# Performance work log

Measured on AMD Instinct MI355X. Metric: run time of the kernel, lower is better.

## Reference

```python
import jax, jax.numpy as jnp
import numpy as np

# FalconMamba2 SSM decoder layer: RMSNorm -> Mamba2 mixer (in_proj, causal depthwise
# conv + SiLU, chunked SSD scan, gated RMSNorm, out_proj) -> residual add.
H_DIM = 2048      # hidden_size
D_SSM = 4096      # mamba_expand * hidden_size
NH = 64           # num heads
P = 64            # head_dim = D_SSM // NH
G = 1             # n_groups
N = 128           # ssm state size
K = 4             # conv kernel
CS = 256          # chunk size
EPS = 1e-5


def rmsnorm(x, w, eps=EPS):
    v = jnp.mean(jnp.square(x), axis=-1, keepdims=True)
    return x * jax.lax.rsqrt(v + eps) * w


def setup_inputs() -> dict:
    key = jax.random.key(0)
    ks = jax.random.split(key, 8)
    proj_dim = 2 * D_SSM + 2 * G * N + NH   # 8512
    conv_dim = D_SSM + 2 * G * N            # 4352
    s = 0.02
    return {
        "x": jax.random.normal(ks[0], (1, 2048, H_DIM), jnp.float32),
        "rms_w": jnp.ones((H_DIM,), jnp.float32),
        "W_in": jax.random.normal(ks[1], (proj_dim, H_DIM), jnp.float32) * s,
        "conv_w": jax.random.normal(ks[2], (conv_dim, K), jnp.float32) * 0.2,
        "conv_b": jnp.zeros((conv_dim,), jnp.float32),
        "dt_bias": jax.random.uniform(ks[3], (NH,), jnp.float32,
                                      minval=float(np.log(1e-3)), maxval=float(np.log(0.1))),
        "A_log": jnp.log(jax.random.uniform(ks[4], (NH,), jnp.float32, minval=1.0, maxval=16.0)),
        "D": jax.random.normal(ks[5], (NH,), jnp.float32) * 0.1 + 1.0,
        "norm_w": jnp.ones((D_SSM,), jnp.float32),
        "W_out": jax.random.normal(ks[6], (H_DIM, D_SSM), jnp.float32) * s,
    }


def reference(x, rms_w, W_in, conv_w, conv_b, dt_bias, A_log, D, norm_w, W_out):
    Bsz, L, _ = x.shape
    h = rmsnorm(x, rms_w)                                   # input_layernorm
    proj = jnp.einsum('blh,ph->blp', h, W_in)               # in_proj (no bias)
    z, xBC, dt = jnp.split(proj, [D_SSM, 2 * D_SSM + 2 * G * N], axis=-1)

    # causal depthwise conv1d (kernel K) + SiLU
    xp = jnp.pad(xBC, ((0, 0), (K - 1, 0), (0, 0)))
    xc = conv_b + sum(xp[:, k:k + L, :] * conv_w[:, k] for k in range(K))
    xc = jax.nn.silu(xc)
    xs, Bm, Cm = jnp.split(xc, [D_SSM, D_SSM + G * N], axis=-1)

    dt = jax.nn.softplus(dt + dt_bias)                      # [B,L,NH]
    A = -jnp.exp(A_log)                                     # [NH]

    nc = L // CS
    xs = xs.reshape(Bsz, nc, CS, NH, P)
    Bm = Bm.reshape(Bsz, nc, CS, G, N)
    Cm = Cm.reshape(Bsz, nc, CS, G, N)
    dtc = dt.reshape(Bsz, nc, CS, NH)

    dA = dtc * A                                            # [B,c,l,h]
    dAc = jnp.cumsum(dA, axis=2)
    dAh = jnp.moveaxis(dAc, 3, 2)                           # [B,c,h,l]
    dth = jnp.moveaxis(dtc, 3, 2)                           # [B,c,h,l]

    # intra-chunk (diagonal block) output
    seg = dAh[..., :, None] - dAh[..., None, :]             # [B,c,h,l,s]
    tril = jnp.tril(jnp.ones((CS, CS), bool))
    Lmat = jnp.exp(jnp.where(tril, seg, -jnp.inf))
    CB = jnp.einsum('bclgn,bcsgn->bcls', Cm, Bm)            # G=1 shared across heads
    M = CB[:, :, None] * Lmat * dth[..., None, :]           # [B,c,h,l,s]
    Y_diag = jnp.einsum('bchls,bcshp->bclhp', M, xs)

    # per-chunk final states and inter-chunk recurrence
    decay_states = jnp.exp(dAh[..., -1:] - dAh)             # [B,c,h,l]
    states = jnp.einsum('bclgn,bchl,bclhp->bchpn', Bm, decay_states * dth, xs)
    chunk_decay = jnp.exp(dAh[..., -1])                     # [B,c,h]

    def step(carry, inp):
        dec, st = inp
        return carry * dec[..., None, None] + st, carry     # emit state BEFORE chunk

    st_t = jnp.moveaxis(states, 1, 0)                       # [c,B,h,p,n]
    dec_t = jnp.moveaxis(chunk_decay, 1, 0)                 # [c,B,h]
    _, prev_states = jax.lax.scan(step, jnp.zeros_like(st_t[0]), (dec_t, st_t))
    prev_states = jnp.moveaxis(prev_states, 0, 1)           # [B,c,h,p,n]

    Y_off = jnp.einsum('bclgn,bchpn,bchl->bclhp', Cm, prev_states, jnp.exp(dAh))

    y = (Y_diag + Y_off + xs * D[:, None]).reshape(Bsz, L, D_SSM)
    y = rmsnorm(y * jax.nn.silu(z), norm_w)                 # gated RMSNorm
    out = jnp.einsum('bld,hd->blh', y, W_out)               # out_proj
    return x + out                                          # residual
```

## Files before the change

### kernel.cpp

```cpp
#include <hip/hip_runtime.h>
#include <stdint.h>


typedef __bf16 bf16x8 __attribute__((ext_vector_type(8)));
typedef float  f32x4  __attribute__((ext_vector_type(4)));

#define DEVFN __device__ __forceinline__

DEVFN unsigned short f2b(float f) {
  uint32_t u = __builtin_bit_cast(uint32_t, f);
  u += 0x7fffu + ((u >> 16) & 1u);
  return (unsigned short)(u >> 16);
}
DEVFN float b2f(unsigned short u) {
  uint32_t x = (uint32_t)u << 16;
  return __builtin_bit_cast(float, x);
}
DEVFN bf16x8 pack8(const float (&m)[8]) {
  bf16x8 r;
#pragma unroll
  for (int t = 0; t < 8; ++t) r[t] = (__bf16)m[t];
  return r;
}

DEVFN void tile_map(int bid, int nwg, int nm, int nn, int grp, int& mt, int& nt) {
  const int q = nwg >> 3, r = nwg & 7;
  const int xcd = bid & 7, lid = bid >> 3;
  const int wg = (xcd < r ? xcd * (q + 1) : r * (q + 1) + (xcd - r) * q) + lid;
  const int per = grp * nn;
  const int g = wg / per;
  const int rem = wg - g * per;
  const int lim = nm - g * grp;
  const int gm = lim < grp ? lim : grp;
  mt = g * grp + rem % gm;
  nt = rem / gm;
}

__global__ void f32_to_bf16_two(
    const float* __restrict__ s1, unsigned short* __restrict__ d1,
    long src1, long dst1,
    const float* __restrict__ s2, unsigned short* __restrict__ d2,
    long src2, long dst2) {
  long i = ((long)blockIdx.x * 256 + threadIdx.x) * 4;
  const float* s; unsigned short* d; long srcE;
  if (i < dst1) { s = s1; d = d1; srcE = src1; }
  else {
    i -= dst1;
    if (i >= dst2) return;
    s = s2; d = d2; srcE = src2;
  }
  ushort4 o;
  if (i < srcE) {
    float4 v = *reinterpret_cast<const float4*>(s + i);
    o.x = f2b(v.x); o.y = f2b(v.y); o.z = f2b(v.z); o.w = f2b(v.w);
  } else {
    o.x = 0; o.y = 0; o.z = 0; o.w = 0;
  }
  *reinterpret_cast<ushort4*>(d + i) = o;
}

__global__ __launch_bounds__(256) void rmsnorm_in(
    const float* __restrict__ x, const float* __restrict__ w,
    unsigned short* __restrict__ h) {
  const int row = blockIdx.x;
  const int base = threadIdx.x * 8;
  if (row >= 2048) {
    ushort4 z = {0, 0, 0, 0};
    *reinterpret_cast<ushort4*>(h + (size_t)row * 2048 + base)     = z;
    *reinterpret_cast<ushort4*>(h + (size_t)row * 2048 + base + 4) = z;
    return;
  }
  const float* xr = x + (size_t)row * 2048;
  float4 v0 = *reinterpret_cast<const float4*>(xr + base);
  float4 v1 = *reinterpret_cast<const float4*>(xr + base + 4);
  float ss = v0.x*v0.x + v0.y*v0.y + v0.z*v0.z + v0.w*v0.w
           + v1.x*v1.x + v1.y*v1.y + v1.z*v1.z + v1.w*v1.w;
  __shared__ float red[4];
#pragma unroll
  for (int off = 32; off > 0; off >>= 1) ss += __shfl_xor(ss, off);
  if ((threadIdx.x & 63) == 0) red[threadIdx.x >> 6] = ss;
  __syncthreads();
  ss = red[0] + red[1] + red[2] + red[3];
  const float scale = rsqrtf(ss * (1.0f / 2048.0f) + 1e-5f);
  float vals[8] = {v0.x, v0.y, v0.z, v0.w, v1.x, v1.y, v1.z, v1.w};
  unsigned short o[8];
#pragma unroll
  for (int j = 0; j < 8; ++j) o[j] = f2b(vals[j] * scale * w[base + j]);
  ushort4 a, b;
  a.x = o[0]; a.y = o[1]; a.z = o[2]; a.w = o[3];
  b.x = o[4]; b.y = o[5]; b.z = o[6]; b.w = o[7];
  *reinterpret_cast<ushort4*>(h + (size_t)row * 2048 + base)     = a;
  *reinterpret_cast<ushort4*>(h + (size_t)row * 2048 + base + 4) = b;
}

template<int BM, bool RES>
__global__ __launch_bounds__(256, 2) void gemm_pipe(
    const unsigned short* __restrict__ A, const unsigned short* __restrict__ B,
    float* __restrict__ C, const float* __restrict__ res,
    int K, int Mc, int Nc, int ldc, int nm, int nn, int grp) {
  constexpr int MF = BM / 32;
  __shared__ __align__(16) unsigned short As[2][BM * 64];
  __shared__ __align__(16) unsigned short Bs[2][128 * 64];
  int mt, nt;
  tile_map(blockIdx.x, nm * nn, nm, nn, grp, mt, nt);
  const int m0 = mt * BM;
  const int n0 = nt * 128;
  const int tid  = threadIdx.x;
  const int wid  = tid >> 6;
  const int lane = tid & 63;
  const int wm   = (wid >> 1) * (BM / 2);
  const int wn   = (wid & 1) * 64;
  const int lrow = lane & 15;
  const int lkc  = lane >> 4;

  auto stageA = [&](int buf, int k0) {
#pragma unroll
    for (int i = 0; i < MF; ++i) {
      const int ci = tid + i * 256;
      const int r = ci >> 3, cc = ci & 7;
      const int gc = cc ^ (r & 7);
      __builtin_amdgcn_global_load_lds(
          (const __attribute__((address_space(1))) void*)(A + (size_t)(m0 + r) * K + k0 + gc * 8),
          (__attribute__((address_space(3))) void*)(&As[buf][ci * 8]), 16, 0, 0);
    }
  };
  auto stageB = [&](int buf, int k0) {
#pragma unroll
    for (int i = 0; i < 4; ++i) {
      const int ci = tid + i * 256;
      const int r = ci >> 3, cc = ci & 7;
      const int gc = cc ^ (r & 7);
      __builtin_amdgcn_global_load_lds(
          (const __attribute__((address_space(1))) void*)(B + (size_t)(n0 + r) * K + k0 + gc * 8),
          (__attribute__((address_space(3))) void*)(&Bs[buf][ci * 8]), 16, 0, 0);
    }
  };

  f32x4 acc[MF][4] = {};
  const int nsteps = K >> 6;

  stageA(0, 0); stageB(0, 0);
  if (nsteps > 1) { stageA(1, 64); stageB(1, 64); }
  if (nsteps > 1) asm volatile("s_waitcnt vmcnt(%0)" :: "n"(MF + 4) : "memory");
  else            asm volatile("s_waitcnt vmcnt(0)" ::: "memory");
  __builtin_amdgcn_s_barrier();
  __builtin_amdgcn_sched_barrier(0);

  int cur = 0;
  for (int t = 0; t < nsteps; ++t) {
    bf16x8 af[MF][2], bf[4][2];
#pragma unroll
    for (int m = 0; m < MF; ++m)
#pragma unroll
      for (int kk = 0; kk < 2; ++kk) {
        const int row = wm + m * 16 + lrow;
        const int c = kk * 4 + lkc;
        af[m][kk] = *reinterpret_cast<const bf16x8*>(
            &As[cur][row * 64 + ((c ^ (row & 7)) * 8)]);
      }
#pragma unroll
    for (int n = 0; n < 4; ++n)
#pragma unroll
      for (int kk = 0; kk < 2; ++kk) {
        const int row = wn + n * 16 + lrow;
        const int c = kk * 4 + lkc;
        bf[n][kk] = *reinterpret_cast<const bf16x8*>(
            &Bs[cur][row * 64 + ((c ^ (row & 7)) * 8)]);
      }
    asm volatile("s_waitcnt lgkmcnt(0)" ::: "memory");
    __builtin_amdgcn_sched_barrier(0);
    __builtin_amdgcn_s_barrier();
    if (t + 2 < nsteps) { stageA(cur, (t + 2) * 64); stageB(cur, (t + 2) * 64); }
    __builtin_amdgcn_s_setprio(1);
#pragma unroll
    for (int kk = 0; kk < 2; ++kk)
#pragma unroll
      for (int m = 0; m < MF; ++m)
#pragma unroll
        for (int n = 0; n < 4; ++n)
          acc[m][n] = __builtin_amdgcn_mfma_f32_16x16x32_bf16(af[m][kk], bf[n][kk], acc[m][n], 0, 0, 0);
    __builtin_amdgcn_s_setprio(0);
    if (t + 1 < nsteps) {
      if (t + 2 < nsteps) asm volatile("s_waitcnt vmcnt(%0)" :: "n"(MF + 4) : "memory");
      else                asm volatile("s_waitcnt vmcnt(0)" ::: "memory");
      __builtin_amdgcn_sched_barrier(0);
      __builtin_amdgcn_s_barrier();
    }
    cur ^= 1;
  }

#pragma unroll
  for (int m = 0; m < MF; ++m) {
#pragma unroll
    for (int n = 0; n < 4; ++n) {
      const int col = n0 + wn + n * 16 + lrow;
      if (col < Nc) {
#pragma unroll
        for (int v = 0; v < 4; ++v) {
          const int row = m0 + wm + m * 16 + (lane >> 4) * 4 + v;
          if (row < Mc) {
            const size_t idx = (size_t)row * ldc + col;
            float val = acc[m][n][v];
            if (RES) val += res[idx];
            C[idx] = val;
          }
        }
      }
    }
  }
}

template<int BM, bool RES>
__global__ __launch_bounds__(256, 2) void gemm_pipe3(
    const unsigned short* __restrict__ A, const unsigned short* __restrict__ B,
    float* __restrict__ C, const float* __restrict__ res,
    int K, int Mc, int Nc, int ldc, int nm, int nn, int grp) {
  constexpr int MF = BM / 32;
  constexpr int LPS = MF + 4;
  __shared__ __align__(16) unsigned short As[3][BM * 64];
  __shared__ __align__(16) unsigned short Bs[3][128 * 64];
  int mt, nt;
  tile_map(blockIdx.x, nm * nn, nm, nn, grp, mt, nt);
  const int m0 = mt * BM;
  const int n0 = nt * 128;
  const int tid  = threadIdx.x;
  const int wid  = tid >> 6;
  const int lane = tid & 63;
  const int wm   = (wid >> 1) * (BM / 2);
  const int wn   = (wid & 1) * 64;
  const int lrow = lane & 15;
  const int lkc  = lane >> 4;

  auto stage = [&](int buf, int k0) {
#pragma unroll
    for (int i = 0; i < MF; ++i) {
      const int ci = tid + i * 256;
      const int r = ci >> 3, cc = ci & 7;
      const int gc = cc ^ (r & 7);
      __builtin_amdgcn_global_load_lds(
          (const __attribute__((address_space(1))) void*)(A + (size_t)(m0 + r) * K + k0 + gc * 8),
          (__attribute__((address_space(3))) void*)(&As[buf][ci * 8]), 16, 0, 0);
    }
#pragma unroll
    for (int i = 0; i < 4; ++i) {
      const int ci = tid + i * 256;
      const int r = ci >> 3, cc = ci & 7;
      const int gc = cc ^ (r & 7);
      __builtin_amdgcn_global_load_lds(
          (const __attribute__((address_space(1))) void*)(B + (size_t)(n0 + r) * K + k0 + gc * 8),
          (__attribute__((address_space(3))) void*)(&Bs[buf][ci * 8]), 16, 0, 0);
    }
  };

  f32x4 acc[MF][4] = {};
  const int nsteps = K >> 6;

  stage(0, 0);
  if (nsteps > 1) stage(1, 64);
  if (nsteps > 2) stage(2, 128);
  if (nsteps > 2)      asm volatile("s_waitcnt vmcnt(%0)" :: "n"(2 * LPS) : "memory");
  else if (nsteps > 1) asm volatile("s_waitcnt vmcnt(%0)" :: "n"(LPS) : "memory");
  else                 asm volatile("s_waitcnt vmcnt(0)" ::: "memory");
  __builtin_amdgcn_s_barrier();
  __builtin_amdgcn_sched_barrier(0);

  int cur = 0;
  for (int t = 0; t < nsteps; ++t) {
    bf16x8 af[MF][2], bf[4][2];
#pragma unroll
    for (int m = 0; m < MF; ++m)
#pragma unroll
      for (int kk = 0; kk < 2; ++kk) {
        const int row = wm + m * 16 + lrow;
        const int c = kk * 4 + lkc;
        af[m][kk] = *reinterpret_cast<const bf16x8*>(
            &As[cur][row * 64 + ((c ^ (row & 7)) * 8)]);
      }
#pragma unroll
    for (int n = 0; n < 4; ++n)
#pragma unroll
      for (int kk = 0; kk < 2; ++kk) {
        const int row = wn + n * 16 + lrow;
        const int c = kk * 4 + lkc;
        bf[n][kk] = *reinterpret_cast<const bf16x8*>(
            &Bs[cur][row * 64 + ((c ^ (row & 7)) * 8)]);
      }
    asm volatile("s_waitcnt lgkmcnt(0)" ::: "memory");
    __builtin_amdgcn_sched_barrier(0);
    __builtin_amdgcn_s_barrier();
    if (t + 3 < nsteps) stage(cur, (t + 3) * 64);
    __builtin_amdgcn_s_setprio(1);
#pragma unroll
    for (int kk = 0; kk < 2; ++kk)
#pragma unroll
      for (int m = 0; m < MF; ++m)
#pragma unroll
        for (int n = 0; n < 4; ++n)
          acc[m][n] = __builtin_amdgcn_mfma_f32_16x16x32_bf16(af[m][kk], bf[n][kk], acc[m][n], 0, 0, 0);
    __builtin_amdgcn_s_setprio(0);
    if (t + 1 < nsteps) {
      if (t + 3 < nsteps)      asm volatile("s_waitcnt vmcnt(%0)" :: "n"(2 * LPS) : "memory");
      else if (t + 2 < nsteps) asm volatile("s_waitcnt vmcnt(%0)" :: "n"(LPS) : "memory");
      else                     asm volatile("s_waitcnt vmcnt(0)" ::: "memory");
      __builtin_amdgcn_sched_barrier(0);
      __builtin_amdgcn_s_barrier();
    }
    cur = (cur == 2) ? 0 : cur + 1;
  }

#pragma unroll
  for (int m = 0; m < MF; ++m) {
#pragma unroll
    for (int n = 0; n < 4; ++n) {
      const int col = n0 + wn + n * 16 + lrow;
      if (col < Nc) {
#pragma unroll
        for (int v = 0; v < 4; ++v) {
          const int row = m0 + wm + m * 16 + (lane >> 4) * 4 + v;
          if (row < Mc) {
            const size_t idx = (size_t)row * ldc + col;
            float val = acc[m][n][v];
            if (RES) val += res[idx];
            C[idx] = val;
          }
        }
      }
    }
  }
}

__global__ __launch_bounds__(256) void conv_silu_dt(
    const float* __restrict__ proj, const float* __restrict__ conv_w,
    const float* __restrict__ conv_b, const float* __restrict__ dt_bias,
    unsigned short* __restrict__ xs, float* __restrict__ BC,
    unsigned short* __restrict__ BTb, unsigned short* __restrict__ Bsb,
    unsigned short* __restrict__ Cbb, float* __restrict__ dtc) {
  const int cch = blockIdx.x * 256 + threadIdx.x;
  const int l0 = blockIdx.y * 16;
  if (cch < 4352) {
    const float4 w = *reinterpret_cast<const float4*>(conv_w + (size_t)cch * 4);
    const float b = conv_b[cch];
    const float* pcol = proj + 4096 + cch;
    float w0, w1, w2;
    w0 = (l0 >= 3) ? pcol[(size_t)(l0 - 3) * 8512] : 0.0f;
    w1 = (l0 >= 2) ? pcol[(size_t)(l0 - 2) * 8512] : 0.0f;
    w2 = (l0 >= 1) ? pcol[(size_t)(l0 - 1) * 8512] : 0.0f;
#pragma unroll
    for (int i = 0; i < 16; ++i) {
      const int l = l0 + i;
      const float cur = pcol[(size_t)l * 8512];
      float acc = b + w0 * w.x + w1 * w.y + w2 * w.z + cur * w.w;
      w0 = w1; w1 = w2; w2 = cur;
      acc = acc / (1.0f + __expf(-acc));
      if (cch < 4096) {
        xs[(size_t)l * 4096 + cch] = f2b(acc);
      } else {
        BC[(size_t)l * 256 + (cch - 4096)] = acc;
        if (cch < 4224) {
          const int n = cch - 4096;
          const unsigned short bb = f2b(acc);
          BTb[((size_t)((l >> 8) * 128) + n) * 256 + (l & 255)] = bb;
          Bsb[(size_t)l * 128 + n] = bb;
        } else {
          const int n = cch - 4224;
          Cbb[(size_t)l * 128 + n] = f2b(acc);
        }
      }
    }
  } else if (cch < 4416) {
    const int hh = cch - 4352;
    const float bias = dt_bias[hh];
#pragma unroll
    for (int i = 0; i < 16; ++i) {
      const int l = l0 + i;
      const float v = proj[(size_t)l * 8512 + 8448 + hh] + bias;
      dtc[(size_t)l * 64 + hh] = (v > 20.0f) ? v : log1pf(expf(v));
    }
  }
}

__global__ __launch_bounds__(256) void cb_mfma(
    const unsigned short* __restrict__ Cbb,
    const unsigned short* __restrict__ Bsb,
    float* __restrict__ CB) {
  const int bx = blockIdx.x;
  const int c = bx >> 3;
  const int l0 = (bx & 7) * 32;
  const int tid = threadIdx.x;
  const int wid = tid >> 6;
  const int lane = tid & 63;
  const int wm = (wid >> 1) * 16;
  const int wn = (wid & 1) * 128;
  const int lrow = lane & 15;
  const int lk = (lane >> 4) * 8;
  const size_t arow = (size_t)(c * 256 + l0 + wm + lrow) * 128;
  f32x4 acc[8] = {};
#pragma unroll
  for (int kk = 0; kk < 4; ++kk) {
    bf16x8 av = *reinterpret_cast<const bf16x8*>(Cbb + arow + kk * 32 + lk);
#pragma unroll
    for (int nf = 0; nf < 8; ++nf) {
      bf16x8 bv = *reinterpret_cast<const bf16x8*>(
          Bsb + (size_t)(c * 256 + wn + nf * 16 + lrow) * 128 + kk * 32 + lk);
      acc[nf] = __builtin_amdgcn_mfma_f32_16x16x32_bf16(av, bv, acc[nf], 0, 0, 0);
    }
  }
#pragma unroll
  for (int nf = 0; nf < 8; ++nf) {
    const int s = wn + nf * 16 + lrow;
#pragma unroll
    for (int v = 0; v < 4; ++v) {
      const int l = l0 + wm + (lane >> 4) * 4 + v;
      CB[((size_t)(c * 256) + l) * 256 + s] = acc[nf][v];
    }
  }
}

__global__ __launch_bounds__(512) void ssd_states_scan(
    const unsigned short* __restrict__ xs, const unsigned short* __restrict__ BTb,
    const float* __restrict__ dtc, const float* __restrict__ A_log,
    float* __restrict__ dAc, float* __restrict__ cdec,
    float* __restrict__ statesT) {
  const int bx = blockIdx.x;
  const int c = bx >> 6, h = bx & 63;
  __shared__ __align__(16) unsigned short xwT[64 * 264];
  __shared__ float dAL[256], dtL[256];
  const int tid = threadIdx.x;
  const int lane = tid & 63;
  const int w = tid >> 6;

  if (tid < 256) dtL[tid] = dtc[(size_t)(c * 256 + tid) * 64 + h];
  const float Ah = -__expf(A_log[h]);
  __syncthreads();
  if (tid < 256) dAL[tid] = dtL[tid] * Ah;
  __syncthreads();
  for (int off = 1; off < 256; off <<= 1) {
    const float t = (tid < 256 && tid >= off) ? dAL[tid - off] : 0.0f;
    __syncthreads();
    if (tid < 256) dAL[tid] += t;
    __syncthreads();
  }
  if (tid < 256) dAc[(size_t)bx * 256 + tid] = dAL[tid];
  if (tid == 255) cdec[bx] = __expf(dAL[255]);
  if (tid < 256) dtL[tid] = __expf(dAL[255] - dAL[tid]) * dtL[tid];
  __syncthreads();

#pragma unroll
  for (int it = 0; it < 4; ++it) {
    const int gid = it * 512 + tid;
    const int p = gid & 63;
    const int s0 = (gid >> 6) * 8;
    bf16x8 r;
#pragma unroll
    for (int k = 0; k < 8; ++k)
      r[k] = (__bf16)(b2f(xs[(size_t)(c * 256 + s0 + k) * 4096 + h * 64 + p]) * dtL[s0 + k]);
    *reinterpret_cast<bf16x8*>(&xwT[p * 264 + s0]) = r;
  }
  __syncthreads();

  const int pb = (w & 3) * 16;
  const int nb = (w >> 2) * 64;
  const int kcol = (lane >> 4) * 8;
  f32x4 acc[4] = {};
  for (int k = 0; k < 8; ++k) {
    bf16x8 av = *reinterpret_cast<const bf16x8*>(&xwT[(pb + (lane & 15)) * 264 + k * 32 + kcol]);
#pragma unroll
    for (int nf = 0; nf < 4; ++nf) {
      bf16x8 bv = *reinterpret_cast<const bf16x8*>(
          BTb + ((size_t)(c * 128) + nb + nf * 16 + (lane & 15)) * 256 + k * 32 + kcol);
      acc[nf] = __builtin_amdgcn_mfma_f32_16x16x32_bf16(av, bv, acc[nf], 0, 0, 0);
    }
  }
  const int rb = (lane >> 4) * 4;
#pragma unroll
  for (int nf = 0; nf < 4; ++nf) {
    const int n = nb + nf * 16 + (lane & 15);
#pragma unroll
    for (int v = 0; v < 4; ++v) {
      const int p = pb + rb + v;
      statesT[(size_t)bx * 8192 + p * 128 + n] = acc[nf][v];
    }
  }
}

__global__ void ssd_scan(const float* __restrict__ statesT,
                         unsigned short* __restrict__ prevb,
                         const float* __restrict__ cdec) {
  const int i = blockIdx.x * 256 + threadIdx.x;
  const int h = i >> 13;
  const int r = i & 8191;
  float carry = 0.0f;
#pragma unroll
  for (int c = 0; c < 8; ++c) {
    const size_t idx = ((size_t)(c * 64 + h)) * 8192 + r;
    const float st = statesT[idx];
    prevb[idx] = f2b(carry);
    carry = carry * cdec[c * 64 + h] + st;
  }
}

__global__ __launch_bounds__(512) void ssd_diag_off(
    const unsigned short* xs, const float* __restrict__ BC,
    const float* __restrict__ dtc, const float* __restrict__ dAc,
    const float* __restrict__ CB, const unsigned short* __restrict__ prevb,
    const float* __restrict__ Dp, unsigned short* y) {
  const int bx = blockIdx.x;
  const int c = bx >> 6, h = bx & 63;
  __shared__ __align__(16) unsigned short xsT[64 * 264];
  __shared__ float dAL[256], dtL[256], vdt[256];
  const int tid = threadIdx.x;
  const int lane = tid & 63;
  const int w = tid >> 6;

  if (tid < 256) {
    dAL[tid] = dAc[(size_t)bx * 256 + tid];
    dtL[tid] = dtc[(size_t)(c * 256 + tid) * 64 + h];
  }
  __syncthreads();
  if (tid < 256) vdt[tid] = __expf(dAL[tid | 31] - dAL[tid]) * dtL[tid];
#pragma unroll
  for (int it = 0; it < 4; ++it) {
    const int gid = it * 512 + tid;
    const int p = gid & 63;
    const int s0 = (gid >> 6) * 8;
    unsigned short r[8];
#pragma unroll
    for (int k = 0; k < 8; ++k)
      r[k] = xs[(size_t)(c * 256 + s0 + k) * 4096 + h * 64 + p];
    *reinterpret_cast<uint4*>(&xsT[p * 264 + s0]) = *reinterpret_cast<uint4*>(r);
  }
  __syncthreads();

  const int l1 = w * 32 + (lane & 15);
  const int l2 = l1 + 16;
  const int kcol = (lane >> 4) * 8;
  const float dA1 = dAL[l1], dA2 = dAL[l2];
  const float* CBr1 = CB + ((size_t)(c * 256) + l1) * 256;
  const float* CBr2 = CB + ((size_t)(c * 256) + l2) * 256;
  f32x4 acc[2][4] = {};

  for (int j = 0; j < w; ++j) {
    const int s0 = j * 32 + kcol;
    float cb1[8], cb2[8];
    *reinterpret_cast<float4*>(&cb1[0]) = *reinterpret_cast<const float4*>(CBr1 + s0);
    *reinterpret_cast<float4*>(&cb1[4]) = *reinterpret_cast<const float4*>(CBr1 + s0 + 4);
    *reinterpret_cast<float4*>(&cb2[0]) = *reinterpret_cast<const float4*>(CBr2 + s0);
    *reinterpret_cast<float4*>(&cb2[4]) = *reinterpret_cast<const float4*>(CBr2 + s0 + 4);
    const float a = dAL[j * 32 + 31];
    const float u1 = __expf(dA1 - a), u2 = __expf(dA2 - a);
    float m1[8], m2[8];
#pragma unroll
    for (int t = 0; t < 8; ++t) {
      const float uv = vdt[s0 + t];
      m1[t] = cb1[t] * (u1 * uv);
      m2[t] = cb2[t] * (u2 * uv);
    }
    bf16x8 a1 = pack8(m1), a2 = pack8(m2);
#pragma unroll
    for (int nf = 0; nf < 4; ++nf) {
      bf16x8 bv = *reinterpret_cast<const bf16x8*>(
          &xsT[(nf * 16 + (lane & 15)) * 264 + j * 32 + kcol]);
      acc[0][nf] = __builtin_amdgcn_mfma_f32_16x16x32_bf16(a1, bv, acc[0][nf], 0, 0, 0);
      acc[1][nf] = __builtin_amdgcn_mfma_f32_16x16x32_bf16(a2, bv, acc[1][nf], 0, 0, 0);
    }
  }
  {
    const int s0 = w * 32 + kcol;
    float cb1[8], cb2[8];
    *reinterpret_cast<float4*>(&cb1[0]) = *reinterpret_cast<const float4*>(CBr1 + s0);
    *reinterpret_cast<float4*>(&cb1[4]) = *reinterpret_cast<const float4*>(CBr1 + s0 + 4);
    *reinterpret_cast<float4*>(&cb2[0]) = *reinterpret_cast<const float4*>(CBr2 + s0);
    *reinterpret_cast<float4*>(&cb2[4]) = *reinterpret_cast<const float4*>(CBr2 + s0 + 4);
    float m1[8], m2[8];
#pragma unroll
    for (int t = 0; t < 8; ++t) {
      const int s = s0 + t;
      const float e1 = __expf(fminf(dA1 - dAL[s], 0.0f)) * dtL[s];
      const float e2 = __expf(fminf(dA2 - dAL[s], 0.0f)) * dtL[s];
      m1[t] = (s <= l1) ? cb1[t] * e1 : 0.0f;
      m2[t] = (s <= l2) ? cb2[t] * e2 : 0.0f;
    }
    bf16x8 a1 = pack8(m1), a2 = pack8(m2);
#pragma unroll
    for (int nf = 0; nf < 4; ++nf) {
      bf16x8 bv = *reinterpret_cast<const bf16x8*>(
          &xsT[(nf * 16 + (lane & 15)) * 264 + w * 32 + kcol]);
      acc[0][nf] = __builtin_amdgcn_mfma_f32_16x16x32_bf16(a1, bv, acc[0][nf], 0, 0, 0);
      acc[1][nf] = __builtin_amdgcn_mfma_f32_16x16x32_bf16(a2, bv, acc[1][nf], 0, 0, 0);
    }
  }
  {
    const float eA1 = __expf(dA1), eA2 = __expf(dA2);
    const float* Cr1 = BC + ((size_t)(c * 256) + l1) * 256 + 128;
    const float* Cr2 = BC + ((size_t)(c * 256) + l2) * 256 + 128;
    const unsigned short* pv = prevb + (size_t)bx * 8192;
#pragma unroll
    for (int q = 0; q < 4; ++q) {
      const int n0 = q * 32 + kcol;
      float c1[8], c2[8];
      *reinterpret_cast<float4*>(&c1[0]) = *reinterpret_cast<const float4*>(Cr1 + n0);
      *reinterpret_cast<float4*>(&c1[4]) = *reinterpret_cast<const float4*>(Cr1 + n0 + 4);
      *reinterpret_cast<float4*>(&c2[0]) = *reinterpret_cast<const float4*>(Cr2 + n0);
      *reinterpret_cast<float4*>(&c2[4]) = *reinterpret_cast<const float4*>(Cr2 + n0 + 4);
      float m1[8], m2[8];
#pragma unroll
      for (int t = 0; t < 8; ++t) { m1[t] = c1[t] * eA1; m2[t] = c2[t] * eA2; }
      bf16x8 a1 = pack8(m1), a2 = pack8(m2);
#pragma unroll
      for (int nf = 0; nf < 4; ++nf) {
        bf16x8 bv = *reinterpret_cast<const bf16x8*>(
            pv + (size_t)(nf * 16 + (lane & 15)) * 128 + n0);
        acc[0][nf] = __builtin_amdgcn_mfma_f32_16x16x32_bf16(a1, bv, acc[0][nf], 0, 0, 0);
        acc[1][nf] = __builtin_amdgcn_mfma_f32_16x16x32_bf16(a2, bv, acc[1][nf], 0, 0, 0);
      }
    }
  }
  const float Dh = Dp[h];
  const int rb = (lane >> 4) * 4;
#pragma unroll
  for (int mf = 0; mf < 2; ++mf) {
#pragma unroll
    for (int nf = 0; nf < 4; ++nf) {
      const int p = nf * 16 + (lane & 15);
#pragma unroll
      for (int v = 0; v < 4; ++v) {
        const int l = w * 32 + mf * 16 + rb + v;
        y[(size_t)(c * 256 + l) * 4096 + h * 64 + p] =
            f2b(acc[mf][nf][v] + Dh * b2f(xsT[p * 264 + l]));
      }
    }
  }
}

__global__ __launch_bounds__(256) void gated_rmsnorm(
    const unsigned short* __restrict__ y, const float* __restrict__ proj,
    const float* __restrict__ nw, unsigned short* __restrict__ y2) {
  const int row = blockIdx.x;
  const unsigned short* yr = y + (size_t)row * 4096;
  const float* zr = proj + (size_t)row * 8512;
  const int base = threadIdx.x * 16;
  unsigned short yu[16];
  *reinterpret_cast<uint4*>(&yu[0]) = *reinterpret_cast<const uint4*>(yr + base);
  *reinterpret_cast<uint4*>(&yu[8]) = *reinterpret_cast<const uint4*>(yr + base + 8);
  float g[16];
  float ss = 0.0f;
#pragma unroll
  for (int j = 0; j < 16; j += 4) {
    const float4 zv = *reinterpret_cast<const float4*>(zr + base + j);
    const float a0 = b2f(yu[j])     * (zv.x / (1.0f + expf(-zv.x)));
    const float a1 = b2f(yu[j + 1]) * (zv.y / (1.0f + expf(-zv.y)));
    const float a2 = b2f(yu[j + 2]) * (zv.z / (1.0f + expf(-zv.z)));
    const float a3 = b2f(yu[j + 3]) * (zv.w / (1.0f + expf(-zv.w)));
    g[j] = a0; g[j+1] = a1; g[j+2] = a2; g[j+3] = a3;
    ss += a0*a0 + a1*a1 + a2*a2 + a3*a3;
  }
  __shared__ float red[4];
#pragma unroll
  for (int off = 32; off > 0; off >>= 1) ss += __shfl_xor(ss, off);
  if ((threadIdx.x & 63) == 0) red[threadIdx.x >> 6] = ss;
  __syncthreads();
  ss = red[0] + red[1] + red[2] + red[3];
  const float scale = rsqrtf(ss * (1.0f / 4096.0f) + 1e-5f);
#pragma unroll
  for (int j = 0; j < 16; j += 4) {
    ushort4 o;
    o.x = f2b(g[j]   * scale * nw[base + j]);
    o.y = f2b(g[j+1] * scale * nw[base + j + 1]);
    o.z = f2b(g[j+2] * scale * nw[base + j + 2]);
    o.w = f2b(g[j+3] * scale * nw[base + j + 3]);
    *reinterpret_cast<ushort4*>(y2 + (size_t)row * 4096 + base + j) = o;
  }
}

extern "C" void kernel_launch(void* const* d_in, const int* in_sizes, int n_in,
                              void* d_out, int out_size, void* d_ws, size_t ws_size,
                              hipStream_t stream) {
  const float* x       = (const float*)d_in[0];
  const float* rms_w   = (const float*)d_in[1];
  const float* W_in    = (const float*)d_in[2];
  const float* conv_w  = (const float*)d_in[3];
  const float* conv_b  = (const float*)d_in[4];
  const float* dt_bias = (const float*)d_in[5];
  const float* A_log   = (const float*)d_in[6];
  const float* Dp      = (const float*)d_in[7];
  const float* norm_w  = (const float*)d_in[8];
  const float* W_out   = (const float*)d_in[9];
  float* out = (float*)d_out;

  char* ws = (char*)d_ws;
  size_t off = 0;
  auto alloc = [&](size_t bytes) {
    void* p = ws + off;
    off += (bytes + 255) & ~(size_t)255;
    return p;
  };
  unsigned short* Wb_in  = (unsigned short*)alloc((size_t)8576 * 2048 * 2);
  unsigned short* Wb_out = (unsigned short*)alloc((size_t)2048 * 4096 * 2);
  unsigned short* hbuf   = (unsigned short*)alloc((size_t)2112 * 2048 * 2);
  float* proj   = (float*)alloc((size_t)2048 * 8512 * 4);
  unsigned short* xsbuf = (unsigned short*)alloc((size_t)2048 * 4096 * 2);
  float* BCbuf  = (float*)alloc((size_t)2048 * 256 * 4);
  unsigned short* BTb = (unsigned short*)alloc((size_t)8 * 128 * 256 * 2);
  unsigned short* Bsb = (unsigned short*)alloc((size_t)2048 * 128 * 2);
  unsigned short* Cbb = (unsigned short*)alloc((size_t)2048 * 128 * 2);
  float* dtcbuf = (float*)alloc((size_t)2048 * 64 * 4);
  float* dAcbuf = (float*)alloc((size_t)512 * 256 * 4);
  float* cdec   = (float*)alloc((size_t)512 * 4);
  float* CBbuf  = (float*)alloc((size_t)8 * 256 * 256 * 4);
  float* statesT = (float*)alloc((size_t)512 * 64 * 128 * 4);
  unsigned short* y2 = Wb_in;
  unsigned short* prevb = hbuf;

  (void)in_sizes; (void)n_in; (void)out_size; (void)ws_size;

  {
    const long d1 = (long)8576 * 2048, s1 = (long)8512 * 2048;
    const long d2 = (long)2048 * 4096, s2 = d2;
    const long chunks = (d1 + d2) / 4;
    f32_to_bf16_two<<<(int)((chunks + 255) / 256), 256, 0, stream>>>(
        W_in, Wb_in, s1, d1, W_out, Wb_out, s2, d2);
  }

  rmsnorm_in<<<2112, 256, 0, stream>>>(x, rms_w, hbuf);

  gemm_pipe<192, false><<<11 * 67, 256, 0, stream>>>(hbuf, Wb_in, proj, nullptr,
                                                     2048, 2048, 8512, 8512,
                                                     11, 67, 4);

  conv_silu_dt<<<dim3(18, 128), 256, 0, stream>>>(proj, conv_w, conv_b, dt_bias,
                                                  xsbuf, BCbuf, BTb, Bsb, Cbb,
                                                  dtcbuf);

  cb_mfma<<<64, 256, 0, stream>>>(Cbb, Bsb, CBbuf);

  ssd_states_scan<<<512, 512, 0, stream>>>(xsbuf, BTb, dtcbuf, A_log,
                                           dAcbuf, cdec, statesT);

  ssd_scan<<<2048, 256, 0, stream>>>(statesT, prevb, cdec);

  ssd_diag_off<<<512, 512, 0, stream>>>(xsbuf, BCbuf, dtcbuf, dAcbuf, CBbuf,
                                        prevb, Dp, xsbuf);

  gated_rmsnorm<<<2048, 256, 0, stream>>>(xsbuf, proj, norm_w, y2);

  gemm_pipe3<64, true><<<32 * 16, 256, 0, stream>>>(y2, Wb_out, out, x,
                                                    4096, 2048, 2048, 2048,
                                                    32, 16, 4);
}
```

Baseline: 267.9 us.

## Store in_proj output as bf16 and fuse small kernels into neighbors

The in_proj GEMM now writes its projection in bf16 instead of fp32. The conv/dt and gated RMSNorm kernels read that bf16 buffer, which halves traffic on the largest intermediate. Weight conversion and the input RMSNorm are merged into one launch, and the C·B MFMA kernel is folded into the states kernel as extra blocks, cutting launch overhead. The cost is reduced precision for z, xBC and dt before the softplus and conv.

```diff
diff --git a/kernel.cpp b/kernel.cpp
--- a/kernel.cpp
+++ b/kernel.cpp
@@ -36,33 +36,33 @@
   nt = rem / gm;
 }
 
-__global__ void f32_to_bf16_two(
-    const float* __restrict__ s1, unsigned short* __restrict__ d1,
-    long src1, long dst1,
-    const float* __restrict__ s2, unsigned short* __restrict__ d2,
-    long src2, long dst2) {
-  long i = ((long)blockIdx.x * 256 + threadIdx.x) * 4;
-  const float* s; unsigned short* d; long srcE;
-  if (i < dst1) { s = s1; d = d1; srcE = src1; }
-  else {
-    i -= dst1;
-    if (i >= dst2) return;
-    s = s2; d = d2; srcE = src2;
-  }
-  ushort4 o;
-  if (i < srcE) {
-    float4 v = *reinterpret_cast<const float4*>(s + i);
-    o.x = f2b(v.x); o.y = f2b(v.y); o.z = f2b(v.z); o.w = f2b(v.w);
-  } else {
-    o.x = 0; o.y = 0; o.z = 0; o.w = 0;
-  }
-  *reinterpret_cast<ushort4*>(d + i) = o;
-}
-
-__global__ __launch_bounds__(256) void rmsnorm_in(
-    const float* __restrict__ x, const float* __restrict__ w,
-    unsigned short* __restrict__ h) {
-  const int row = blockIdx.x;
+__global__ __launch_bounds__(256) void prep(
+    const float* __restrict__ W_in, unsigned short* __restrict__ Wb_in,
+    const float* __restrict__ W_out, unsigned short* __restrict__ Wb_out,
+    const float* __restrict__ x, const float* __restrict__ rms_w,
+    unsigned short* __restrict__ h, int ncvt) {
+  const long d1 = (long)8576 * 2048, s1 = (long)8512 * 2048;
+  const long d2 = (long)2048 * 4096;
+  if (blockIdx.x < (unsigned)ncvt) {
+    long i = ((long)blockIdx.x * 256 + threadIdx.x) * 4;
+    const float* s; unsigned short* d; long srcE;
+    if (i < d1) { s = W_in; d = Wb_in; srcE = s1; }
+    else {
+      i -= d1;
+      if (i >= d2) return;
+      s = W_out; d = Wb_out; srcE = d2;
+    }
+    ushort4 o;
+    if (i < srcE) {
+      float4 v = *reinterpret_cast<const float4*>(s + i);
+      o.x = f2b(v.x); o.y = f2b(v.y); o.z = f2b(v.z); o.w = f2b(v.w);
+    } else {
+      o.x = 0; o.y = 0; o.z = 0; o.w = 0;
+    }
+    *reinterpret_cast<ushort4*>(d + i) = o;
+    return;
+  }
+  const int row = blockIdx.x - ncvt;
   const int base = threadIdx.x * 8;
   if (row >= 2048) {
     ushort4 z = {0, 0, 0, 0};
@@ -85,7 +85,7 @@
   float vals[8] = {v0.x, v0.y, v0.z, v0.w, v1.x, v1.y, v1.z, v1.w};
   unsigned short o[8];
 #pragma unroll
-  for (int j = 0; j < 8; ++j) o[j] = f2b(vals[j] * scale * w[base + j]);
+  for (int j = 0; j < 8; ++j) o[j] = f2b(vals[j] * scale * rms_w[base + j]);
   ushort4 a, b;
   a.x = o[0]; a.y = o[1]; a.z = o[2]; a.w = o[3];
   b.x = o[4]; b.y = o[5]; b.z = o[6]; b.w = o[7];
@@ -93,10 +93,10 @@
   *reinterpret_cast<ushort4*>(h + (size_t)row * 2048 + base + 4) = b;
 }
 
-template<int BM, bool RES>
+template<int BM, bool RES, bool OUT16>
 __global__ __launch_bounds__(256, 2) void gemm_pipe(
     const unsigned short* __restrict__ A, const unsigned short* __restrict__ B,
-    float* __restrict__ C, const float* __restrict__ res,
+    void* __restrict__ Cv, const float* __restrict__ res,
     int K, int Mc, int Nc, int ldc, int nm, int nn, int grp) {
   constexpr int MF = BM / 32;
   __shared__ __align__(16) unsigned short As[2][BM * 64];
@@ -201,8 +201,12 @@
           if (row < Mc) {
             const size_t idx = (size_t)row * ldc + col;
             float val = acc[m][n][v];
-            if (RES) val += res[idx];
-            C[idx] = val;
+            if constexpr (OUT16) {
+              ((unsigned short*)Cv)[idx] = f2b(val);
+            } else {
+              if (RES) val += res[idx];
+              ((float*)Cv)[idx] = val;
+            }
           }
         }
       }
@@ -330,7 +334,7 @@
 }
 
 __global__ __launch_bounds__(256) void conv_silu_dt(
-    const float* __restrict__ proj, const float* __restrict__ conv_w,
+    const unsigned short* __restrict__ proj, const float* __restrict__ conv_w,
     const float* __restrict__ conv_b, const float* __restrict__ dt_bias,
     unsigned short* __restrict__ xs, float* __restrict__ BC,
     unsigned short* __restrict__ BTb, unsigned short* __restrict__ Bsb,
@@ -340,15 +344,15 @@
   if (cch < 4352) {
     const float4 w = *reinterpret_cast<const float4*>(conv_w + (size_t)cch * 4);
     const float b = conv_b[cch];
-    const float* pcol = proj + 4096 + cch;
+    const unsigned short* pcol = proj + 4096 + cch;
     float w0, w1, w2;
-    w0 = (l0 >= 3) ? pcol[(size_t)(l0 - 3) * 8512] : 0.0f;
-    w1 = (l0 >= 2) ? pcol[(size_t)(l0 - 2) * 8512] : 0.0f;
-    w2 = (l0 >= 1) ? pcol[(size_t)(l0 - 1) * 8512] : 0.0f;
+    w0 = (l0 >= 3) ? b2f(pcol[(size_t)(l0 - 3) * 8512]) : 0.0f;
+    w1 = (l0 >= 2) ? b2f(pcol[(size_t)(l0 - 2) * 8512]) : 0.0f;
+    w2 = (l0 >= 1) ? b2f(pcol[(size_t)(l0 - 1) * 8512]) : 0.0f;
 #pragma unroll
     for (int i = 0; i < 16; ++i) {
       const int l = l0 + i;
-      const float cur = pcol[(size_t)l * 8512];
+      const float cur = b2f(pcol[(size_t)l * 8512]);
       float acc = b + w0 * w.x + w1 * w.y + w2 * w.z + cur * w.w;
       w0 = w1; w1 = w2; w2 = cur;
       acc = acc / (1.0f + __expf(-acc));
@@ -373,61 +377,59 @@
 #pragma unroll
     for (int i = 0; i < 16; ++i) {
       const int l = l0 + i;
-      const float v = proj[(size_t)l * 8512 + 8448 + hh] + bias;
+      const float v = b2f(proj[(size_t)l * 8512 + 8448 + hh]) + bias;
       dtc[(size_t)l * 64 + hh] = (v > 20.0f) ? v : log1pf(expf(v));
     }
   }
 }
 
-__global__ __launch_bounds__(256) void cb_mfma(
-    const unsigned short* __restrict__ Cbb,
-    const unsigned short* __restrict__ Bsb,
-    float* __restrict__ CB) {
-  const int bx = blockIdx.x;
-  const int c = bx >> 3;
-  const int l0 = (bx & 7) * 32;
-  const int tid = threadIdx.x;
-  const int wid = tid >> 6;
-  const int lane = tid & 63;
-  const int wm = (wid >> 1) * 16;
-  const int wn = (wid & 1) * 128;
-  const int lrow = lane & 15;
-  const int lk = (lane >> 4) * 8;
-  const size_t arow = (size_t)(c * 256 + l0 + wm + lrow) * 128;
-  f32x4 acc[8] = {};
-#pragma unroll
-  for (int kk = 0; kk < 4; ++kk) {
-    bf16x8 av = *reinterpret_cast<const bf16x8*>(Cbb + arow + kk * 32 + lk);
-#pragma unroll
-    for (int nf = 0; nf < 8; ++nf) {
-      bf16x8 bv = *reinterpret_cast<const bf16x8*>(
-          Bsb + (size_t)(c * 256 + wn + nf * 16 + lrow) * 128 + kk * 32 + lk);
-      acc[nf] = __builtin_amdgcn_mfma_f32_16x16x32_bf16(av, bv, acc[nf], 0, 0, 0);
-    }
-  }
-#pragma unroll
-  for (int nf = 0; nf < 8; ++nf) {
-    const int s = wn + nf * 16 + lrow;
-#pragma unroll
-    for (int v = 0; v < 4; ++v) {
-      const int l = l0 + wm + (lane >> 4) * 4 + v;
-      CB[((size_t)(c * 256) + l) * 256 + s] = acc[nf][v];
-    }
-  }
-}
-
-__global__ __launch_bounds__(512) void ssd_states_scan(
+__global__ __launch_bounds__(512) void ssd_states_scan_cb(
     const unsigned short* __restrict__ xs, const unsigned short* __restrict__ BTb,
     const float* __restrict__ dtc, const float* __restrict__ A_log,
     float* __restrict__ dAc, float* __restrict__ cdec,
-    float* __restrict__ statesT) {
+    float* __restrict__ statesT,
+    const unsigned short* __restrict__ Cbb, const unsigned short* __restrict__ Bsb,
+    float* __restrict__ CB) {
+  const int tid = threadIdx.x;
+  const int lane = tid & 63;
+  const int w = tid >> 6;
+
+  if (blockIdx.x >= 512) {
+    const int bx2 = blockIdx.x - 512;
+    const int c = bx2 >> 2;
+    const int l0 = (bx2 & 3) * 64;
+    const int wm = (w >> 1) * 16;
+    const int wn = (w & 1) * 128;
+    const int lrow = lane & 15;
+    const int lk = (lane >> 4) * 8;
+    const size_t arow = (size_t)(c * 256 + l0 + wm + lrow) * 128;
+    f32x4 acc[8] = {};
+#pragma unroll
+    for (int kk = 0; kk < 4; ++kk) {
+      bf16x8 av = *reinterpret_cast<const bf16x8*>(Cbb + arow + kk * 32 + lk);
+#pragma unroll
+      for (int nf = 0; nf < 8; ++nf) {
+        bf16x8 bv = *reinterpret_cast<const bf16x8*>(
+            Bsb + (size_t)(c * 256 + wn + nf * 16 + lrow) * 128 + kk * 32 + lk);
+        acc[nf] = __builtin_amdgcn_mfma_f32_16x16x32_bf16(av, bv, acc[nf], 0, 0, 0);
+      }
+    }
+#pragma unroll
+    for (int nf = 0; nf < 8; ++nf) {
+      const int s = wn + nf * 16 + lrow;
+#pragma unroll
+      for (int v = 0; v < 4; ++v) {
+        const int l = l0 + wm + (lane >> 4) * 4 + v;
+        CB[((size_t)(c * 256) + l) * 256 + s] = acc[nf][v];
+      }
+    }
+    return;
+  }
+
   const int bx = blockIdx.x;
   const int c = bx >> 6, h = bx & 63;
   __shared__ __align__(16) unsigned short xwT[64 * 264];
   __shared__ float dAL[256], dtL[256];
-  const int tid = threadIdx.x;
-  const int lane = tid & 63;
-  const int w = tid >> 6;
 
   if (tid < 256) dtL[tid] = dtc[(size_t)(c * 256 + tid) * 64 + h];
   const float Ah = -__expf(A_log[h]);
@@ -633,26 +635,25 @@
 }
 
 __global__ __launch_bounds__(256) void gated_rmsnorm(
-    const unsigned short* __restrict__ y, const float* __restrict__ proj,
+    const unsigned short* __restrict__ y, const unsigned short* __restrict__ proj,
     const float* __restrict__ nw, unsigned short* __restrict__ y2) {
   const int row = blockIdx.x;
   const unsigned short* yr = y + (size_t)row * 4096;
-  const float* zr = proj + (size_t)row * 8512;
+  const unsigned short* zr = proj + (size_t)row * 8512;
   const int base = threadIdx.x * 16;
-  unsigned short yu[16];
+  unsigned short yu[16], zu[16];
   *reinterpret_cast<uint4*>(&yu[0]) = *reinterpret_cast<const uint4*>(yr + base);
   *reinterpret_cast<uint4*>(&yu[8]) = *reinterpret_cast<const uint4*>(yr + base + 8);
+  *reinterpret_cast<uint4*>(&zu[0]) = *reinterpret_cast<const uint4*>(zr + base);
+  *reinterpret_cast<uint4*>(&zu[8]) = *reinterpret_cast<const uint4*>(zr + base + 8);
   float g[16];
   float ss = 0.0f;
 #pragma unroll
-  for (int j = 0; j < 16; j += 4) {
-    const float4 zv = *reinterpret_cast<const float4*>(zr + base + j);
-    const float a0 = b2f(yu[j])     * (zv.x / (1.0f + expf(-zv.x)));
-    const float a1 = b2f(yu[j + 1]) * (zv.y / (1.0f + expf(-zv.y)));
-    const float a2 = b2f(yu[j + 2]) * (zv.z / (1.0f + expf(-zv.z)));
-    const float a3 = b2f(yu[j + 3]) * (zv.w / (1.0f + expf(-zv.w)));
-    g[j] = a0; g[j+1] = a1; g[j+2] = a2; g[j+3] = a3;
-    ss += a0*a0 + a1*a1 + a2*a2 + a3*a3;
+  for (int j = 0; j < 16; ++j) {
+    const float zf = b2f(zu[j]);
+    const float a = b2f(yu[j]) * (zf / (1.0f + expf(-zf)));
+    g[j] = a;
+    ss += a * a;
   }
   __shared__ float red[4];
 #pragma unroll
@@ -697,8 +698,8 @@
   unsigned short* Wb_in  = (unsigned short*)alloc((size_t)8576 * 2048 * 2);
   unsigned short* Wb_out = (unsigned short*)alloc((size_t)2048 * 4096 * 2);
   unsigned short* hbuf   = (unsigned short*)alloc((size_t)2112 * 2048 * 2);
-  float* proj   = (float*)alloc((size_t)2048 * 8512 * 4);
-  unsigned short* xsbuf = (unsigned short*)alloc((size_t)2048 * 4096 * 2);
+  unsigned short* proj   = (unsigned short*)alloc((size_t)2048 * 8512 * 2);
+  unsigned short* xsbuf  = (unsigned short*)alloc((size_t)2048 * 4096 * 2);
   float* BCbuf  = (float*)alloc((size_t)2048 * 256 * 4);
   unsigned short* BTb = (unsigned short*)alloc((size_t)8 * 128 * 256 * 2);
   unsigned short* Bsb = (unsigned short*)alloc((size_t)2048 * 128 * 2);
@@ -713,28 +714,21 @@
 
   (void)in_sizes; (void)n_in; (void)out_size; (void)ws_size;
 
-  {
-    const long d1 = (long)8576 * 2048, s1 = (long)8512 * 2048;
-    const long d2 = (long)2048 * 4096, s2 = d2;
-    const long chunks = (d1 + d2) / 4;
-    f32_to_bf16_two<<<(int)((chunks + 255) / 256), 256, 0, stream>>>(
-        W_in, Wb_in, s1, d1, W_out, Wb_out, s2, d2);
-  }
-
-  rmsnorm_in<<<2112, 256, 0, stream>>>(x, rms_w, hbuf);
-
-  gemm_pipe<192, false><<<11 * 67, 256, 0, stream>>>(hbuf, Wb_in, proj, nullptr,
-                                                     2048, 2048, 8512, 8512,
-                                                     11, 67, 4);
+  const long cvtChunks = ((long)8576 * 2048 + (long)2048 * 4096) / 4;
+  const int ncvt = (int)((cvtChunks + 255) / 256);
+  prep<<<ncvt + 2112, 256, 0, stream>>>(W_in, Wb_in, W_out, Wb_out,
+                                        x, rms_w, hbuf, ncvt);
+
+  gemm_pipe<192, false, true><<<11 * 67, 256, 0, stream>>>(
+      hbuf, Wb_in, proj, nullptr, 2048, 2048, 8512, 8512, 11, 67, 4);
 
   conv_silu_dt<<<dim3(18, 128), 256, 0, stream>>>(proj, conv_w, conv_b, dt_bias,
                                                   xsbuf, BCbuf, BTb, Bsb, Cbb,
                                                   dtcbuf);
 
-  cb_mfma<<<64, 256, 0, stream>>>(Cbb, Bsb, CBbuf);
-
-  ssd_states_scan<<<512, 512, 0, stream>>>(xsbuf, BTb, dtcbuf, A_log,
-                                           dAcbuf, cdec, statesT);
+  ssd_states_scan_cb<<<544, 512, 0, stream>>>(xsbuf, BTb, dtcbuf, A_log,
+                                              dAcbuf, cdec, statesT,
+                                              Cbb, Bsb, CBbuf);
 
   ssd_scan<<<2048, 256, 0, stream>>>(statesT, prevb, cdec);
 
```

Result: no change. 262.7 us, median of 2 (-1.9%).
